# Kernel tuning notes

Measured on AMD Instinct MI355X. Metric: run time of the kernel, lower is better.

Reference implementation:

```python
import jax, jax.numpy as jnp
import numpy as np

N = 50000       # nodes
E = 800000      # edges (before self-loops)
IN_DIM = 128
HID = 16
H1 = 8
OUT_DIM = 16
H2 = 1
NEG_SLOPE = 0.2  # PyG GATConv LeakyReLU negative slope


def setup_inputs() -> dict:
    key = jax.random.key(0)
    ks = jax.random.split(key, 10)
    x = jax.random.normal(ks[0], (N, IN_DIM), dtype=jnp.float32)
    edge_index = jax.random.randint(ks[1], (2, E), 0, N, dtype=jnp.int32)
    # layer 1: Linear(IN_DIM -> H1*HID, no bias), att vectors [H, C], bias [H1*HID]
    W1 = jax.random.normal(ks[2], (IN_DIM, H1 * HID), dtype=jnp.float32) / np.sqrt(IN_DIM).astype(np.float32)
    a_src1 = jax.random.normal(ks[3], (H1, HID), dtype=jnp.float32) * 0.1
    a_dst1 = jax.random.normal(ks[4], (H1, HID), dtype=jnp.float32) * 0.1
    b1 = jnp.zeros((H1 * HID,), dtype=jnp.float32)
    # layer 2: Linear(H1*HID -> H2*OUT_DIM), concat=False -> bias [OUT_DIM]
    W2 = jax.random.normal(ks[5], (H1 * HID, H2 * OUT_DIM), dtype=jnp.float32) / np.sqrt(H1 * HID).astype(np.float32)
    a_src2 = jax.random.normal(ks[6], (H2, OUT_DIM), dtype=jnp.float32) * 0.1
    a_dst2 = jax.random.normal(ks[7], (H2, OUT_DIM), dtype=jnp.float32) * 0.1
    b2 = jnp.zeros((OUT_DIM,), dtype=jnp.float32)
    return {"x": x, "edge_index": edge_index, "W1": W1, "a_src1": a_src1,
            "a_dst1": a_dst1, "b1": b1, "W2": W2, "a_src2": a_src2,
            "a_dst2": a_dst2, "b2": b2}


def gat_conv(x, src, dst, W, a_src, a_dst, bias, heads, ch, concat):
    n = x.shape[0]
    h = (x @ W).reshape(n, heads, ch)                      # [N,H,C]
    s_src = jnp.sum(h * a_src, axis=-1)                    # [N,H] att_src . Wx
    s_dst = jnp.sum(h * a_dst, axis=-1)                    # [N,H]
    e = jax.nn.leaky_relu(s_src[src] + s_dst[dst], NEG_SLOPE)  # [Etot,H]
    # segment softmax over incoming edges per target node
    m = jax.ops.segment_max(e, dst, num_segments=n)        # [N,H]
    ee = jnp.exp(e - m[dst])
    denom = jax.ops.segment_sum(ee, dst, num_segments=n)   # [N,H]
    alpha = ee / denom[dst]                                # [Etot,H]
    out = jax.ops.segment_sum(h[src] * alpha[:, :, None], dst, num_segments=n)  # [N,H,C]
    out = out.reshape(n, heads * ch) if concat else out.mean(axis=1)
    return out + bias


def reference(x, edge_index, W1, a_src1, a_dst1, b1, W2, a_src2, a_dst2, b2):
    n = x.shape[0]
    loop = jnp.arange(n, dtype=edge_index.dtype)           # PyG adds self-loops
    src = jnp.concatenate([edge_index[0], loop])
    dst = jnp.concatenate([edge_index[1], loop])
    # eval mode: F.dropout is identity
    h = jax.nn.elu(gat_conv(x, src, dst, W1, a_src1, a_dst1, b1, H1, HID, True))
    out = gat_conv(h, src, dst, W2, a_src2, a_dst2, b2, H2, OUT_DIM, False)
    return jax.nn.log_softmax(out, axis=1)
```

## Files before the change

kernel.cpp:

```cpp
#include <hip/hip_runtime.h>
#include <hip/hip_fp16.h>
#include <math.h>

#define NEG_SLOPE 0.2f
#define MAXDEG 64
#define CSTRIDE 16
#define NXCD 8
#define NSLICE 256

typedef short bf16x8 __attribute__((ext_vector_type(8)));
typedef float f32x4 __attribute__((ext_vector_type(4)));

__device__ __forceinline__ unsigned short f2bf(float f) {
    union { float f; unsigned u; } v; v.f = f;
    unsigned r = v.u + 0x7FFF + ((v.u >> 16) & 1);
    return (unsigned short)(r >> 16);
}

__global__ void k_init(const float* __restrict__ W1, unsigned short* __restrict__ frag,
                       int* __restrict__ cursor, unsigned short* __restrict__ csr, int N)
{
    int gid = blockIdx.x * 256 + threadIdx.x;
    if (gid < 16384) {
        int f = gid >> 3, j = gid & 7;
        int kk = f >> 9, c = (f >> 6) & 7, l = f & 63;
        int col = c * 16 + (l & 15);
        int k = kk * 32 + ((l >> 4) << 3) + j;
        frag[gid] = f2bf(W1[k * 128 + col]);
    }
    if (gid < N) {
        cursor[gid * CSTRIDE] = 1;
        csr[gid * MAXDEG] = (unsigned short)gid;
    }
}

__global__ __launch_bounds__(256) void k_mega(
    const float* __restrict__ x, const bf16x8* __restrict__ frag,
    const float* __restrict__ a_src, const float* __restrict__ a_dst,
    __half* __restrict__ h1h, float* __restrict__ ssrc, float* __restrict__ sdst,
    int N, int G1,
    const int* __restrict__ src_e, const int* __restrict__ dst_e, int E,
    int* __restrict__ cursor, unsigned short* __restrict__ csr)
{
    const int t = threadIdx.x;

    if (blockIdx.x >= G1) {
        int fb = blockIdx.x - G1;
        int xcd = blockIdx.x & (NXCD - 1);
        int slice = fb >> 3;
        int dlo = (int)(((long)N * xcd) >> 3);
        int dhi = (int)(((long)N * (xcd + 1)) >> 3);
        int e0 = (int)((long)E * slice / NSLICE);
        int e1 = (int)((long)E * (slice + 1) / NSLICE);
        for (int i = e0 + t; i < e1; i += 256) {
            int d = dst_e[i];
            if (d >= dlo && d < dhi) {
                int s = src_e[i];
                int pos = atomicAdd(&cursor[d * CSTRIDE], 1);
                if (pos < MAXDEG) csr[d * MAXDEG + pos] = (unsigned short)s;
            }
        }
        return;
    }

    const int r0 = blockIdx.x * 64;
    const int w = t >> 6, l = t & 63;
    const int lo = l & 15, hi = l >> 4;
    const int row = r0 + w * 16 + lo;
    const bool rok = (row < N);

    f32x4 acc[8] = {};
    #pragma unroll
    for (int kk = 0; kk < 4; ++kk) {
        bf16x8 a;
        {
            float4 f0 = make_float4(0.f,0.f,0.f,0.f), f1 = f0;
            if (rok) {
                const float4* xp = (const float4*)(x + (size_t)row * 128 + kk * 32 + hi * 8);
                f0 = xp[0]; f1 = xp[1];
            }
            a[0] = (short)f2bf(f0.x); a[1] = (short)f2bf(f0.y);
            a[2] = (short)f2bf(f0.z); a[3] = (short)f2bf(f0.w);
            a[4] = (short)f2bf(f1.x); a[5] = (short)f2bf(f1.y);
            a[6] = (short)f2bf(f1.z); a[7] = (short)f2bf(f1.w);
        }
        #pragma unroll
        for (int c = 0; c < 8; ++c) {
            bf16x8 b = frag[(kk * 8 + c) * 64 + l];
            acc[c] = __builtin_amdgcn_mfma_f32_16x16x32_bf16(a, b, acc[c], 0, 0, 0);
        }
    }

    float av_s[8], av_d[8];
    #pragma unroll
    for (int c = 0; c < 8; ++c) {
        av_s[c] = a_src[c * 16 + lo];
        av_d[c] = a_dst[c * 16 + lo];
    }

    #pragma unroll
    for (int reg = 0; reg < 4; ++reg) {
        int grow = r0 + w * 16 + hi * 4 + reg;
        bool ok = (grow < N);
        if (ok) {
            #pragma unroll
            for (int c = 0; c < 8; ++c)
                h1h[(size_t)grow * 128 + c * 16 + lo] = __float2half(acc[c][reg]);
        }
        #pragma unroll
        for (int c = 0; c < 8; ++c) {
            float ps = acc[c][reg] * av_s[c];
            float pd = acc[c][reg] * av_d[c];
            #pragma unroll
            for (int m = 8; m >= 1; m >>= 1) {
                ps += __shfl_xor(ps, m, 64);
                pd += __shfl_xor(pd, m, 64);
            }
            if (ok && lo == 0) {
                ssrc[grow * 8 + c] = ps;
                sdst[grow * 8 + c] = pd;
            }
        }
    }
}

__global__ __launch_bounds__(256) void k_aggr1g2(
    const int* __restrict__ cursor, const unsigned short* __restrict__ csr,
    const __half2* __restrict__ h1h, const float* __restrict__ ssrc,
    const float* __restrict__ sdst, const float* __restrict__ b1,
    const float* __restrict__ W2, const float* __restrict__ a_src2,
    const float* __restrict__ a_dst2,
    float* __restrict__ h2, float* __restrict__ s2s, float* __restrict__ s2d, int N)
{
    __shared__ float lds_w2[2080];
    __shared__ float lds_h[4][132];
    const int t = threadIdx.x;

    {
        const float4* src = (const float4*)W2;
        #pragma unroll
        for (int i = 0; i < 2; ++i) {
            int f = i * 256 + t;
            ((float4*)lds_w2)[f + ((f >> 7) << 1)] = src[f];
        }
    }
    __syncthreads();

    const int wid = t >> 6;
    const int lane = t & 63;
    const int node = blockIdx.x * 4 + wid;
    if (node >= N) return;
    const int h = lane >> 3;
    const int beg = node * MAXDEG;
    const int end = beg + min(cursor[node * CSTRIDE], MAXDEG);
    const float sd = sdst[node * 8 + h];
    float acc0 = 0.f, acc1 = 0.f, wsum = 0.f;

    int j = beg;
    for (; j + 7 < end; j += 8) {
        int s0 = csr[j],     s1 = csr[j + 1], s2 = csr[j + 2], s3 = csr[j + 3];
        int s4 = csr[j + 4], s5 = csr[j + 5], s6 = csr[j + 6], s7 = csr[j + 7];
        float e0 = ssrc[s0 * 8 + h], e1 = ssrc[s1 * 8 + h];
        float e2 = ssrc[s2 * 8 + h], e3 = ssrc[s3 * 8 + h];
        float e4 = ssrc[s4 * 8 + h], e5 = ssrc[s5 * 8 + h];
        float e6 = ssrc[s6 * 8 + h], e7 = ssrc[s7 * 8 + h];
        __half2 v0 = h1h[(size_t)s0 * 64 + lane];
        __half2 v1 = h1h[(size_t)s1 * 64 + lane];
        __half2 v2 = h1h[(size_t)s2 * 64 + lane];
        __half2 v3 = h1h[(size_t)s3 * 64 + lane];
        __half2 v4 = h1h[(size_t)s4 * 64 + lane];
        __half2 v5 = h1h[(size_t)s5 * 64 + lane];
        __half2 v6 = h1h[(size_t)s6 * 64 + lane];
        __half2 v7 = h1h[(size_t)s7 * 64 + lane];
        e0 += sd; e0 = (e0 >= 0.f) ? e0 : NEG_SLOPE * e0; float w0 = __expf(e0);
        e1 += sd; e1 = (e1 >= 0.f) ? e1 : NEG_SLOPE * e1; float w1 = __expf(e1);
        e2 += sd; e2 = (e2 >= 0.f) ? e2 : NEG_SLOPE * e2; float w2 = __expf(e2);
        e3 += sd; e3 = (e3 >= 0.f) ? e3 : NEG_SLOPE * e3; float w3 = __expf(e3);
        e4 += sd; e4 = (e4 >= 0.f) ? e4 : NEG_SLOPE * e4; float w4 = __expf(e4);
        e5 += sd; e5 = (e5 >= 0.f) ? e5 : NEG_SLOPE * e5; float w5 = __expf(e5);
        e6 += sd; e6 = (e6 >= 0.f) ? e6 : NEG_SLOPE * e6; float w6 = __expf(e6);
        e7 += sd; e7 = (e7 >= 0.f) ? e7 : NEG_SLOPE * e7; float w7 = __expf(e7);
        wsum += ((w0 + w1) + (w2 + w3)) + ((w4 + w5) + (w6 + w7));
        float2 f0 = __half22float2(v0), f1 = __half22float2(v1);
        float2 f2 = __half22float2(v2), f3 = __half22float2(v3);
        float2 f4 = __half22float2(v4), f5 = __half22float2(v5);
        float2 f6 = __half22float2(v6), f7 = __half22float2(v7);
        acc0 = fmaf(w0, f0.x, acc0); acc1 = fmaf(w0, f0.y, acc1);
        acc0 = fmaf(w1, f1.x, acc0); acc1 = fmaf(w1, f1.y, acc1);
        acc0 = fmaf(w2, f2.x, acc0); acc1 = fmaf(w2, f2.y, acc1);
        acc0 = fmaf(w3, f3.x, acc0); acc1 = fmaf(w3, f3.y, acc1);
        acc0 = fmaf(w4, f4.x, acc0); acc1 = fmaf(w4, f4.y, acc1);
        acc0 = fmaf(w5, f5.x, acc0); acc1 = fmaf(w5, f5.y, acc1);
        acc0 = fmaf(w6, f6.x, acc0); acc1 = fmaf(w6, f6.y, acc1);
        acc0 = fmaf(w7, f7.x, acc0); acc1 = fmaf(w7, f7.y, acc1);
    }
    for (; j < end; ++j) {
        int s = csr[j];
        float e = ssrc[s * 8 + h] + sd;
        e = (e >= 0.f) ? e : NEG_SLOPE * e;
        float w = __expf(e);
        wsum += w;
        float2 f = __half22float2(h1h[(size_t)s * 64 + lane]);
        acc0 = fmaf(w, f.x, acc0); acc1 = fmaf(w, f.y, acc1);
    }

    const float2 bb = ((const float2*)b1)[lane];
    float inv = 1.f / wsum;
    float va = acc0 * inv + bb.x;
    float vb = acc1 * inv + bb.y;
    va = (va > 0.f) ? va : expm1f(va);
    vb = (vb > 0.f) ? vb : expm1f(vb);

    {
        int k0 = 2 * lane;
        lds_h[wid][k0 + (k0 >> 5)]     = va;
        lds_h[wid][k0 + 1 + (k0 >> 5)] = vb;
    }
    asm volatile("s_waitcnt lgkmcnt(0)" ::: "memory");
    __builtin_amdgcn_sched_barrier(0);

    const int col = lane & 15, kg = lane >> 4;
    float r = 0.f;
    #pragma unroll
    for (int k2 = 0; k2 < 32; ++k2) {
        int k = kg * 32 + k2;
        int wi = k * 16 + col;
        r = fmaf(lds_h[wid][k + kg], lds_w2[wi + ((wi >> 9) << 3)], r);
    }
    r += __shfl_xor(r, 16, 64);
    r += __shfl_xor(r, 32, 64);
    if (lane < 16) h2[(size_t)node * 16 + col] = r;

    float ps = r * a_src2[col];
    float pd = r * a_dst2[col];
    #pragma unroll
    for (int m = 8; m >= 1; m >>= 1) {
        ps += __shfl_xor(ps, m, 64);
        pd += __shfl_xor(pd, m, 64);
    }
    if (lane == 0) { s2s[node] = ps; s2d[node] = pd; }
}

__global__ __launch_bounds__(256) void k_aggr2(
    const int* __restrict__ cursor, const unsigned short* __restrict__ csr,
    const float* __restrict__ h2, const float* __restrict__ s2s,
    const float* __restrict__ s2d, const float* __restrict__ b2,
    float* __restrict__ out, int N)
{
    int gid = blockIdx.x * 256 + threadIdx.x;
    int node = gid >> 4;
    if (node >= N) return;
    int c = gid & 15;
    const int beg = node * MAXDEG;
    const int end = beg + min(cursor[node * CSTRIDE], MAXDEG);
    float sd = s2d[node];
    float acc = 0.f, wsum = 0.f;

    int j = beg;
    for (; j + 7 < end; j += 8) {
        int s0 = csr[j],     s1 = csr[j + 1], s2 = csr[j + 2], s3 = csr[j + 3];
        int s4 = csr[j + 4], s5 = csr[j + 5], s6 = csr[j + 6], s7 = csr[j + 7];
        float e0 = s2s[s0], e1 = s2s[s1], e2 = s2s[s2], e3 = s2s[s3];
        float e4 = s2s[s4], e5 = s2s[s5], e6 = s2s[s6], e7 = s2s[s7];
        float g0 = h2[(size_t)s0 * 16 + c];
        float g1 = h2[(size_t)s1 * 16 + c];
        float g2 = h2[(size_t)s2 * 16 + c];
        float g3 = h2[(size_t)s3 * 16 + c];
        float g4 = h2[(size_t)s4 * 16 + c];
        float g5 = h2[(size_t)s5 * 16 + c];
        float g6 = h2[(size_t)s6 * 16 + c];
        float g7 = h2[(size_t)s7 * 16 + c];
        e0 += sd; e0 = (e0 >= 0.f) ? e0 : NEG_SLOPE * e0; float w0 = __expf(e0);
        e1 += sd; e1 = (e1 >= 0.f) ? e1 : NEG_SLOPE * e1; float w1 = __expf(e1);
        e2 += sd; e2 = (e2 >= 0.f) ? e2 : NEG_SLOPE * e2; float w2 = __expf(e2);
        e3 += sd; e3 = (e3 >= 0.f) ? e3 : NEG_SLOPE * e3; float w3 = __expf(e3);
        e4 += sd; e4 = (e4 >= 0.f) ? e4 : NEG_SLOPE * e4; float w4 = __expf(e4);
        e5 += sd; e5 = (e5 >= 0.f) ? e5 : NEG_SLOPE * e5; float w5 = __expf(e5);
        e6 += sd; e6 = (e6 >= 0.f) ? e6 : NEG_SLOPE * e6; float w6 = __expf(e6);
        e7 += sd; e7 = (e7 >= 0.f) ? e7 : NEG_SLOPE * e7; float w7 = __expf(e7);
        wsum += ((w0 + w1) + (w2 + w3)) + ((w4 + w5) + (w6 + w7));
        acc = fmaf(w0, g0, acc); acc = fmaf(w1, g1, acc);
        acc = fmaf(w2, g2, acc); acc = fmaf(w3, g3, acc);
        acc = fmaf(w4, g4, acc); acc = fmaf(w5, g5, acc);
        acc = fmaf(w6, g6, acc); acc = fmaf(w7, g7, acc);
    }
    for (; j < end; ++j) {
        int s = csr[j];
        float e = s2s[s] + sd;
        e = (e >= 0.f) ? e : NEG_SLOPE * e;
        float w = __expf(e);
        wsum += w;
        acc = fmaf(w, h2[(size_t)s * 16 + c], acc);
    }

    float v = acc / wsum + b2[c];
    float m = v;
    #pragma unroll
    for (int msk = 8; msk >= 1; msk >>= 1) m = fmaxf(m, __shfl_xor(m, msk, 64));
    float ex = __expf(v - m);
    float sum = ex;
    #pragma unroll
    for (int msk = 8; msk >= 1; msk >>= 1) sum += __shfl_xor(sum, msk, 64);
    out[(size_t)node * 16 + c] = v - m - __logf(sum);
}

extern "C" void kernel_launch(void* const* d_in, const int* in_sizes, int n_in,
                              void* d_out, int out_size, void* d_ws, size_t ws_size,
                              hipStream_t stream)
{
    const float* x      = (const float*)d_in[0];
    const int*   ei     = (const int*)  d_in[1];
    const float* W1     = (const float*)d_in[2];
    const float* a_src1 = (const float*)d_in[3];
    const float* a_dst1 = (const float*)d_in[4];
    const float* b1     = (const float*)d_in[5];
    const float* W2     = (const float*)d_in[6];
    const float* a_src2 = (const float*)d_in[7];
    const float* a_dst2 = (const float*)d_in[8];
    const float* b2     = (const float*)d_in[9];
    float* out = (float*)d_out;

    const int N = in_sizes[0] / 128;
    const int E = in_sizes[1] / 2;
    const int* src_e = ei;
    const int* dst_e = ei + E;

    float* p = (float*)d_ws;
    __half* h1h  = (__half*)p; p += (size_t)N * 64;
    unsigned short* frag = (unsigned short*)p; p += 8192;
    float* ssrc1 = p; p += (size_t)N * 8;
    float* sdst1 = p; p += (size_t)N * 8;
    float* h2    = p; p += (size_t)N * 16;
    float* s2s   = p; p += (size_t)N;
    float* s2d   = p; p += (size_t)N;
    int* ip = (int*)p;
    int* cursor = ip; ip += (size_t)N * CSTRIDE;
    unsigned short* csr = (unsigned short*)ip;

    const int G1 = (N + 63) / 64;
    const int GF = NSLICE * NXCD;

    k_init<<<(N + 255) / 256, 256, 0, stream>>>(W1, frag, cursor, csr, N);

    k_mega<<<G1 + GF, 256, 0, stream>>>(
        x, (const bf16x8*)frag, a_src1, a_dst1, h1h, ssrc1, sdst1, N, G1,
        src_e, dst_e, E, cursor, csr);

    k_aggr1g2<<<(N + 3) / 4, 256, 0, stream>>>(
        cursor, csr, (const __half2*)h1h, ssrc1, sdst1, b1,
        W2, a_src2, a_dst2, h2, s2s, s2d, N);

    k_aggr2<<<((size_t)N * 16 + 255) / 256, 256, 0, stream>>>(
        cursor, csr, h2, s2s, s2d, b2, out, N);
}
```

Before: 130.2 us.

## Pre-bin edges by destination XCD before CSR fill

Adds a binning pass to the prep kernel that packs (src,dst) into one 32-bit word and scatters each edge into one of eight per-XCD buckets, using shared-memory counters plus one global atomic per bucket per block. The fill blocks in the mega kernel then read only their own bucket instead of scanning the whole edge list and discarding most of it. This cuts the edge-list rereads from eight to one, at the cost of an extra pass that writes and reads a packed buffer, a memset, and 16-bit packing that assumes node ids fit in 16 bits.

```diff
diff --git a/kernel.cpp b/kernel.cpp
--- a/kernel.cpp
+++ b/kernel.cpp
@@ -6,7 +6,7 @@
 #define MAXDEG 64
 #define CSTRIDE 16
 #define NXCD 8
-#define NSLICE 256
+#define NS2 128
 
 typedef short bf16x8 __attribute__((ext_vector_type(8)));
 typedef float f32x4 __attribute__((ext_vector_type(4)));
@@ -17,21 +17,46 @@
     return (unsigned short)(r >> 16);
 }
 
-__global__ void k_init(const float* __restrict__ W1, unsigned short* __restrict__ frag,
-                       int* __restrict__ cursor, unsigned short* __restrict__ csr, int N)
-{
-    int gid = blockIdx.x * 256 + threadIdx.x;
-    if (gid < 16384) {
-        int f = gid >> 3, j = gid & 7;
-        int kk = f >> 9, c = (f >> 6) & 7, l = f & 63;
-        int col = c * 16 + (l & 15);
-        int k = kk * 32 + ((l >> 4) << 3) + j;
-        frag[gid] = f2bf(W1[k * 128 + col]);
-    }
-    if (gid < N) {
-        cursor[gid * CSTRIDE] = 1;
-        csr[gid * MAXDEG] = (unsigned short)gid;
-    }
+__global__ __launch_bounds__(256) void k_prep(
+    const float* __restrict__ W1, unsigned short* __restrict__ frag,
+    int* __restrict__ cursor, unsigned short* __restrict__ csr, int N, int Gi,
+    const int* __restrict__ src_e, const int* __restrict__ dst_e, int E,
+    int* __restrict__ gcur, unsigned* __restrict__ binbuf)
+{
+    __shared__ int lcnt[NXCD];
+    __shared__ int lbase[NXCD];
+    const int t = threadIdx.x;
+
+    if (blockIdx.x < Gi) {
+        int gid = blockIdx.x * 256 + t;
+        if (gid < 16384) {
+            int f = gid >> 3, j = gid & 7;
+            int kk = f >> 9, c = (f >> 6) & 7, l = f & 63;
+            int col = c * 16 + (l & 15);
+            int k = kk * 32 + ((l >> 4) << 3) + j;
+            frag[gid] = f2bf(W1[k * 128 + col]);
+        }
+        if (gid < N) {
+            cursor[gid * CSTRIDE] = 1;
+            csr[gid * MAXDEG] = (unsigned short)gid;
+        }
+        return;
+    }
+
+    int i = (blockIdx.x - Gi) * 256 + t;
+    if (t < NXCD) lcnt[t] = 0;
+    __syncthreads();
+    int b = 0, mypos = 0; unsigned pk = 0; bool ok = (i < E);
+    if (ok) {
+        int s = src_e[i], d = dst_e[i];
+        b = (int)(((long)d * NXCD) / N);
+        pk = (unsigned)s | ((unsigned)d << 16);
+        mypos = atomicAdd(&lcnt[b], 1);
+    }
+    __syncthreads();
+    if (t < NXCD) lbase[t] = atomicAdd(&gcur[t], lcnt[t]);
+    __syncthreads();
+    if (ok) binbuf[(size_t)b * E + lbase[b] + mypos] = pk;
 }
 
 __global__ __launch_bounds__(256) void k_mega(
@@ -39,7 +64,7 @@
     const float* __restrict__ a_src, const float* __restrict__ a_dst,
     __half* __restrict__ h1h, float* __restrict__ ssrc, float* __restrict__ sdst,
     int N, int G1,
-    const int* __restrict__ src_e, const int* __restrict__ dst_e, int E,
+    const int* __restrict__ gcur, const unsigned* __restrict__ binbuf, int E,
     int* __restrict__ cursor, unsigned short* __restrict__ csr)
 {
     const int t = threadIdx.x;
@@ -48,17 +73,16 @@
         int fb = blockIdx.x - G1;
         int xcd = blockIdx.x & (NXCD - 1);
         int slice = fb >> 3;
-        int dlo = (int)(((long)N * xcd) >> 3);
-        int dhi = (int)(((long)N * (xcd + 1)) >> 3);
-        int e0 = (int)((long)E * slice / NSLICE);
-        int e1 = (int)((long)E * (slice + 1) / NSLICE);
+        int cnt = gcur[xcd];
+        int e0 = (int)((long)cnt * slice / NS2);
+        int e1 = (int)((long)cnt * (slice + 1) / NS2);
+        const unsigned* bb = binbuf + (size_t)xcd * E;
         for (int i = e0 + t; i < e1; i += 256) {
-            int d = dst_e[i];
-            if (d >= dlo && d < dhi) {
-                int s = src_e[i];
-                int pos = atomicAdd(&cursor[d * CSTRIDE], 1);
-                if (pos < MAXDEG) csr[d * MAXDEG + pos] = (unsigned short)s;
-            }
+            unsigned v = bb[i];
+            int s = (int)(v & 0xffffu);
+            int d = (int)(v >> 16);
+            int pos = atomicAdd(&cursor[d * CSTRIDE], 1);
+            if (pos < MAXDEG) csr[d * MAXDEG + pos] = (unsigned short)s;
         }
         return;
     }
@@ -335,16 +359,24 @@
     float* s2d   = p; p += (size_t)N;
     int* ip = (int*)p;
     int* cursor = ip; ip += (size_t)N * CSTRIDE;
+    int* gcur   = ip; ip += 16;
     unsigned short* csr = (unsigned short*)ip;
-
+    ip += (size_t)N * MAXDEG / 2;
+    unsigned* binbuf = (unsigned*)ip;
+
+    const int Gi = (N + 255) / 256;
+    const int Gb = (E + 255) / 256;
     const int G1 = (N + 63) / 64;
-    const int GF = NSLICE * NXCD;
-
-    k_init<<<(N + 255) / 256, 256, 0, stream>>>(W1, frag, cursor, csr, N);
+    const int GF = NXCD * NS2;
+
+    hipMemsetAsync(gcur, 0, 16 * sizeof(int), stream);
+
+    k_prep<<<Gi + Gb, 256, 0, stream>>>(
+        W1, frag, cursor, csr, N, Gi, src_e, dst_e, E, gcur, binbuf);
 
     k_mega<<<G1 + GF, 256, 0, stream>>>(
         x, (const bf16x8*)frag, a_src1, a_dst1, h1h, ssrc1, sdst1, N, G1,
-        src_e, dst_e, E, cursor, csr);
+        gcur, binbuf, E, cursor, csr);
 
     k_aggr1g2<<<(N + 3) / 4, 256, 0, stream>>>(
         cursor, csr, (const __half2*)h1h, ssrc1, sdst1, b1,
```

Result: slower. 159.7 us (+22.6%).
